# Kernel tuning notes

Measured on AMD Instinct MI355X. Metric: run time of the kernel, lower is better.

Reference implementation:

```python
import jax, jax.numpy as jnp
import numpy as np

V, E, H, L = 16384, 256, 1024, 2  # vocab, edim, rnn_size, layer_depth
B, T, S = 128, 256, 64            # batch, seq_length, nce_samples


def _xavier(k, shape):
    lim = np.sqrt(6.0 / (shape[-2] + shape[-1]))
    return jax.random.uniform(k, shape, jnp.float32, -lim, lim)


def setup_inputs() -> dict:
    key = jax.random.key(0)
    ks = jax.random.split(key, 12)
    return {
        "input_data": jax.random.randint(ks[0], (B, T), 0, V, jnp.int32),
        "targets": jax.random.randint(ks[1], (B, T), 0, V, jnp.int32),
        "nce_samples": jax.random.randint(ks[2], (S,), 0, V, jnp.int32),
        # embedding + input projection (edim != rnn_size path)
        "embedding": _xavier(ks[3], (V, E)),
        "win": _xavier(ks[4], (E, H)),
        "bin_": jnp.zeros((H,), jnp.float32),
        # MI-GRU per-layer params, stacked on leading layer dim L
        "Wxg": _xavier(ks[5], (L, H, 2 * H)),
        "Whg": _xavier(ks[6], (L, H, 2 * H)),
        "ag": jnp.ones((L, 2 * H), jnp.float32),
        "b1g": jnp.full((L, 2 * H), 0.5, jnp.float32),
        "b2g": jnp.full((L, 2 * H), 0.5, jnp.float32),
        "bg": jnp.zeros((L, 2 * H), jnp.float32),
        "Wxc": _xavier(ks[7], (L, H, H)),
        "Whc": _xavier(ks[8], (L, H, H)),
        "ac": jnp.ones((L, H), jnp.float32),
        "b1c": jnp.full((L, H), 0.5, jnp.float32),
        "b2c": jnp.full((L, H), 0.5, jnp.float32),
        "bc": jnp.zeros((L, H), jnp.float32),
        # output / NCE params
        "softmax_w": _xavier(ks[9], (V, H)),
        "softmax_b": jnp.zeros((V,), jnp.float32),
    }


def _mi_gru_stack(x_seq, h0, Wxg, Whg, ag, b1g, b2g, bg, Wxc, Whc, ac, b1c, b2c, bc):
    """x_seq: [T,B,H]; h0: [L,B,H]. Multiplicative-Integration GRU, L layers."""
    nL = h0.shape[0]

    def step(h_all, x_t):
        inp = x_t
        new_h = []
        for l in range(nL):
            h = h_all[l]
            gx = inp @ Wxg[l]                      # [B,2H]
            gh = h @ Whg[l]                        # [B,2H]
            g = jax.nn.sigmoid(ag[l] * gx * gh + b1g[l] * gx + b2g[l] * gh + bg[l])
            r, u = jnp.split(g, 2, axis=-1)        # reset, update gates [B,H]
            cx = inp @ Wxc[l]
            ch = (r * h) @ Whc[l]
            c = jnp.tanh(ac[l] * cx * ch + b1c[l] * cx + b2c[l] * ch + bc[l])
            hn = u * h + (1.0 - u) * c
            new_h.append(hn)
            inp = hn
        return jnp.stack(new_h), inp

    _, outs = jax.lax.scan(step, h0, x_seq)        # outs: [T,B,H] top-layer states
    return outs


def reference(input_data, targets, nce_samples, embedding, win, bin_,
              Wxg, Whg, ag, b1g, b2g, bg, Wxc, Whc, ac, b1c, b2c, bc,
              softmax_w, softmax_b):
    b, t = input_data.shape
    h_dim = win.shape[1]
    # embedding lookup + projection edim -> rnn_size
    emb = embedding[input_data]                            # [B,T,E]
    x = jnp.einsum('bte,eh->bth', emb, win) + bin_         # [B,T,H]
    x_seq = jnp.transpose(x, (1, 0, 2))                    # [T,B,H]
    h0 = jnp.zeros((Wxg.shape[0], b, h_dim), x.dtype)
    outs = _mi_gru_stack(x_seq, h0, Wxg, Whg, ag, b1g, b2g, bg,
                         Wxc, Whc, ac, b1c, b2c, bc)       # [T,B,H]
    out = jnp.transpose(outs, (1, 0, 2)).reshape(-1, h_dim)  # [B*T,H]
    # NCE loss with fixed sampled negatives
    labels = targets.reshape(-1)                           # [B*T]
    true_w = softmax_w[labels]                             # [B*T,H]
    true_logit = jnp.sum(true_w * out, axis=-1) + softmax_b[labels]
    samp_w = softmax_w[nce_samples]                        # [S,H]
    samp_logits = out @ samp_w.T + softmax_b[nce_samples]  # [B*T,S]
    # sigmoid cross-entropy: label 1 for true, 0 for sampled
    loss = jax.nn.softplus(-true_logit) + jnp.sum(jax.nn.softplus(samp_logits), axis=-1)
    cost = jnp.sum(loss) / b / t
    return cost
```

## Files before the change

kernel.cpp:

```cpp
#include <hip/hip_runtime.h>
#include <hip/hip_bf16.h>


#define T_SEQ 256
#define BATCH 128
#define HD    1024

typedef __attribute__((ext_vector_type(8))) short short8v;
typedef __attribute__((ext_vector_type(4))) float f32x4;

static __device__ __forceinline__ short f2b(float v) {
  __hip_bfloat16 h = __float2bfloat16(v);
  return __builtin_bit_cast(short, h);
}
static __device__ __forceinline__ float b2f(short s) {
  return __bfloat162float(__builtin_bit_cast(__hip_bfloat16, s));
}
static __device__ __forceinline__ float sigm(float x) { return 1.f / (1.f + __expf(-x)); }
static __device__ __forceinline__ float splus(float x) {
  return fmaxf(x, 0.f) + log1pf(__expf(-fabsf(x)));
}

struct Acc22 { f32x4 a[2][2]; };

static __device__ __forceinline__ void gemm_wave(
    const short* __restrict__ A, int lda, const short* __restrict__ WT, int ldk,
    int row0, int cb, int K, Acc22& o) {
  const int lane = threadIdx.x & 63;
  const int l15 = lane & 15, g = lane >> 4;
  f32x4 z = {0.f, 0.f, 0.f, 0.f};
  o.a[0][0] = z; o.a[0][1] = z; o.a[1][0] = z; o.a[1][1] = z;
  const short* a0 = A + (size_t)(row0 + l15) * lda + g * 8;
  const short* a1 = a0 + 16 * (size_t)lda;
  const short* b0 = WT + (size_t)(cb + l15) * ldk + g * 8;
  const short* b1 = b0 + 16 * (size_t)ldk;
  for (int k = 0; k < K; k += 32) {
    short8v av0 = *(const short8v*)(a0 + k);
    short8v av1 = *(const short8v*)(a1 + k);
    short8v bv0 = *(const short8v*)(b0 + k);
    short8v bv1 = *(const short8v*)(b1 + k);
    o.a[0][0] = __builtin_amdgcn_mfma_f32_16x16x32_bf16(av0, bv0, o.a[0][0], 0, 0, 0);
    o.a[0][1] = __builtin_amdgcn_mfma_f32_16x16x32_bf16(av0, bv1, o.a[0][1], 0, 0, 0);
    o.a[1][0] = __builtin_amdgcn_mfma_f32_16x16x32_bf16(av1, bv0, o.a[1][0], 0, 0, 0);
    o.a[1][1] = __builtin_amdgcn_mfma_f32_16x16x32_bf16(av1, bv1, o.a[1][1], 0, 0, 0);
  }
}

struct Params {
  const int *tok, *tgt, *nce;
  const float *emb, *win, *binp;
  const float *ag, *b1g, *b2g, *bg, *ac, *b1c, *b2c, *bc;
  const float *smw, *smb;
  short *embB, *winT, *WhgT0, *WhgT1, *WhcT0, *WhcT1, *WXC0T, *WXC1T;
  short *sampWT;
  float *sampb;
  short *X, *OUTb;
  float *h0f, *h1f; short *h0b, *h1b;
  short *rh0b, *rh1b;
  float *u0, *u1, *gh1, *cx1;
  float *gxc0a, *gxc0b;
  float *slog;
  float *dout;
};


__global__ void k_zero(float* __restrict__ p, int n, float* __restrict__ dout) {
  int i = blockIdx.x * 256 + threadIdx.x;
  if (i < n) p[i] = 0.f;
  if (blockIdx.x == 0 && threadIdx.x == 0) *dout = 0.f;
}

__global__ void k_conv(const float* __restrict__ s, short* __restrict__ d, int n) {
  int i = (blockIdx.x * 256 + threadIdx.x) * 4;
  if (i + 4 <= n) {
    float4 v = *(const float4*)(s + i);
    d[i] = f2b(v.x); d[i + 1] = f2b(v.y); d[i + 2] = f2b(v.z); d[i + 3] = f2b(v.w);
  }
}

__global__ void k_transpose(const float* __restrict__ W, short* __restrict__ WT,
                            int K, int N) {
  __shared__ short tile[32][33];
  int nt = blockIdx.x, kt = blockIdx.y;
  int tx = threadIdx.x, ty = threadIdx.y;
#pragma unroll
  for (int r = 0; r < 4; r++) {
    int k = kt * 32 + ty + r * 8;
    int n = nt * 32 + tx;
    tile[ty + r * 8][tx] = f2b(W[(size_t)k * N + n]);
  }
  __syncthreads();
#pragma unroll
  for (int r = 0; r < 4; r++) {
    int n = nt * 32 + ty + r * 8;
    int k = kt * 32 + tx;
    WT[(size_t)n * K + k] = tile[tx][ty + r * 8];
  }
}

__global__ void k_sampw(Params p) {
  int s = blockIdx.x;
  int row = p.nce[s];
  for (int j = threadIdx.x; j < HD; j += 256)
    p.sampWT[s * HD + j] = f2b(p.smw[(size_t)row * HD + j]);
  if (threadIdx.x == 0) p.sampb[s] = p.smb[row];
}

__global__ __launch_bounds__(256) void k_xproj(Params p) {
  int blk = blockIdx.x;
  int mt = blk >> 5, nt = blk & 31;
  int w = threadIdx.x >> 6, lane = threadIdx.x & 63, l15 = lane & 15, g = lane >> 4;
  int row0 = mt * 128 + w * 32, cb = nt * 32;
  const short* ap[2];
#pragma unroll
  for (int mi = 0; mi < 2; mi++) {
    int r = row0 + mi * 16 + l15;
    int tt = r >> 7, bb = r & 127;
    int tk = p.tok[bb * T_SEQ + tt];
    ap[mi] = p.embB + (size_t)tk * 256 + g * 8;
  }
  f32x4 z = {0.f, 0.f, 0.f, 0.f};
  Acc22 acc; acc.a[0][0] = z; acc.a[0][1] = z; acc.a[1][0] = z; acc.a[1][1] = z;
  const short* b0 = p.winT + (size_t)(cb + l15) * 256 + g * 8;
  const short* b1 = b0 + 16 * 256;
  for (int k = 0; k < 256; k += 32) {
    short8v av0 = *(const short8v*)(ap[0] + k);
    short8v av1 = *(const short8v*)(ap[1] + k);
    short8v bv0 = *(const short8v*)(b0 + k);
    short8v bv1 = *(const short8v*)(b1 + k);
    acc.a[0][0] = __builtin_amdgcn_mfma_f32_16x16x32_bf16(av0, bv0, acc.a[0][0], 0, 0, 0);
    acc.a[0][1] = __builtin_amdgcn_mfma_f32_16x16x32_bf16(av0, bv1, acc.a[0][1], 0, 0, 0);
    acc.a[1][0] = __builtin_amdgcn_mfma_f32_16x16x32_bf16(av1, bv0, acc.a[1][0], 0, 0, 0);
    acc.a[1][1] = __builtin_amdgcn_mfma_f32_16x16x32_bf16(av1, bv1, acc.a[1][1], 0, 0, 0);
  }
#pragma unroll
  for (int mi = 0; mi < 2; mi++)
#pragma unroll
    for (int ni = 0; ni < 2; ni++)
#pragma unroll
      for (int i = 0; i < 4; i++) {
        int row = row0 + mi * 16 + g * 4 + i;
        int col = cb + ni * 16 + l15;
        p.X[(size_t)row * HD + col] = f2b(acc.a[mi][ni][i] + p.binp[col]);
      }
}

__global__ __launch_bounds__(256) void k_gxc0init(Params p) {
  int blk = blockIdx.x;
  int w = threadIdx.x >> 6, lane = threadIdx.x & 63, l15 = lane & 15, g = lane >> 4;
  int row0 = w * 32, cb = blk * 32;
  Acc22 acc;
  gemm_wave(p.X, HD, p.WXC0T, HD, row0, cb, HD, acc);
#pragma unroll
  for (int mi = 0; mi < 2; mi++)
#pragma unroll
    for (int ni = 0; ni < 2; ni++)
#pragma unroll
      for (int i = 0; i < 4; i++) {
        int row = row0 + mi * 16 + g * 4 + i;
        int col = cb + ni * 16 + l15;
        p.gxc0a[row * 3072 + col] = acc.a[mi][ni][i];
      }
}


__global__ __launch_bounds__(256) void k_step1(Params p, int t) {
  int blk = blockIdx.x;
  int w = threadIdx.x >> 6, lane = threadIdx.x & 63, l15 = lane & 15, g = lane >> 4;
  int row0 = w * 32;
  bool L0 = blk < 64;
  int cb = (L0 ? blk : blk - 64) * 32;
  const float* gxc = (t & 1) ? p.gxc0b : p.gxc0a;
  Acc22 acc;
  gemm_wave(L0 ? p.h0b : p.h1b, HD, L0 ? p.WhgT0 : p.WhgT1, HD, row0, cb, HD, acc);
#pragma unroll
  for (int mi = 0; mi < 2; mi++)
#pragma unroll
    for (int ni = 0; ni < 2; ni++)
#pragma unroll
      for (int i = 0; i < 4; i++) {
        int row = row0 + mi * 16 + g * 4 + i;
        int col = cb + ni * 16 + l15;
        float gh = acc.a[mi][ni][i];
        if (L0) {
          float gx = gxc[row * 3072 + col];
          float gv = sigm(p.ag[col] * gx * gh + p.b1g[col] * gx + p.b2g[col] * gh + p.bg[col]);
          if (col < HD) p.rh0b[row * HD + col] = f2b(gv * p.h0f[row * HD + col]);
          else          p.u0[row * HD + col - HD] = gv;
        } else {
          p.gh1[row * 2048 + col] = gh;
        }
      }
}

__global__ __launch_bounds__(256) void k_step2(Params p, int t) {
  int blk = blockIdx.x;
  int w = threadIdx.x >> 6, lane = threadIdx.x & 63, l15 = lane & 15, g = lane >> 4;
  int row0 = w * 32, cb = blk * 32;
  const float* gxc = (t & 1) ? p.gxc0b : p.gxc0a;
  Acc22 acc;
  gemm_wave(p.rh0b, HD, p.WhcT0, HD, row0, cb, HD, acc);
#pragma unroll
  for (int mi = 0; mi < 2; mi++)
#pragma unroll
    for (int ni = 0; ni < 2; ni++)
#pragma unroll
      for (int i = 0; i < 4; i++) {
        int row = row0 + mi * 16 + g * 4 + i;
        int col = cb + ni * 16 + l15;
        float ch = acc.a[mi][ni][i];
        float cx = gxc[row * 3072 + 2048 + col];
        float cv = tanhf(p.ac[col] * cx * ch + p.b1c[col] * cx + p.b2c[col] * ch + p.bc[col]);
        float un = p.u0[row * HD + col];
        float ho = p.h0f[row * HD + col];
        float hn = un * ho + (1.f - un) * cv;
        p.h0f[row * HD + col] = hn;
        p.h0b[row * HD + col] = f2b(hn);
      }
}

__global__ __launch_bounds__(256) void k_step3(Params p, int t) {
  int blk = blockIdx.x;
  int w = threadIdx.x >> 6, lane = threadIdx.x & 63, l15 = lane & 15, g = lane >> 4;
  int row0 = w * 32, cb = blk * 32;
  Acc22 acc;
  gemm_wave(p.h0b, HD, p.WXC1T, HD, row0, cb, HD, acc);
#pragma unroll
  for (int mi = 0; mi < 2; mi++)
#pragma unroll
    for (int ni = 0; ni < 2; ni++)
#pragma unroll
      for (int i = 0; i < 4; i++) {
        int row = row0 + mi * 16 + g * 4 + i;
        int col = cb + ni * 16 + l15;
        float v = acc.a[mi][ni][i];
        if (col < 2048) {
          float gh = p.gh1[row * 2048 + col];
          float gv = sigm(p.ag[2048 + col] * v * gh + p.b1g[2048 + col] * v +
                          p.b2g[2048 + col] * gh + p.bg[2048 + col]);
          if (col < HD) p.rh1b[row * HD + col] = f2b(gv * p.h1f[row * HD + col]);
          else          p.u1[row * HD + col - HD] = gv;
        } else {
          p.cx1[row * HD + col - 2048] = v;
        }
      }
}

__global__ __launch_bounds__(256) void k_step4(Params p, int t) {
  int blk = blockIdx.x;
  int w = threadIdx.x >> 6, lane = threadIdx.x & 63, l15 = lane & 15, g = lane >> 4;
  int row0 = w * 32;
  if (blk < 32) {
    int cb = blk * 32;
    Acc22 acc;
    gemm_wave(p.rh1b, HD, p.WhcT1, HD, row0, cb, HD, acc);
#pragma unroll
    for (int mi = 0; mi < 2; mi++)
#pragma unroll
      for (int ni = 0; ni < 2; ni++)
#pragma unroll
        for (int i = 0; i < 4; i++) {
          int row = row0 + mi * 16 + g * 4 + i;
          int col = cb + ni * 16 + l15;
          float ch = acc.a[mi][ni][i];
          float cx = p.cx1[row * HD + col];
          float cv = tanhf(p.ac[HD + col] * cx * ch + p.b1c[HD + col] * cx +
                           p.b2c[HD + col] * ch + p.bc[HD + col]);
          float un = p.u1[row * HD + col];
          float ho = p.h1f[row * HD + col];
          float hn = un * ho + (1.f - un) * cv;
          p.h1f[row * HD + col] = hn;
          p.h1b[row * HD + col] = f2b(hn);
          p.OUTb[((size_t)t * BATCH + row) * HD + col] = f2b(hn);
        }
  } else {
    if (t == T_SEQ - 1) return;
    int cb = (blk - 32) * 32;
    const short* A = p.X + (size_t)(t + 1) * BATCH * HD;
    float* outb = ((t + 1) & 1) ? p.gxc0b : p.gxc0a;
    Acc22 acc;
    gemm_wave(A, HD, p.WXC0T, HD, row0, cb, HD, acc);
#pragma unroll
    for (int mi = 0; mi < 2; mi++)
#pragma unroll
      for (int ni = 0; ni < 2; ni++)
#pragma unroll
        for (int i = 0; i < 4; i++) {
          int row = row0 + mi * 16 + g * 4 + i;
          int col = cb + ni * 16 + l15;
          outb[row * 3072 + col] = acc.a[mi][ni][i];
        }
  }
}


__global__ __launch_bounds__(256) void k_nce_gemm(Params p) {
  int blk = blockIdx.x;
  int mt = blk >> 1, nt = blk & 1;
  int w = threadIdx.x >> 6, lane = threadIdx.x & 63, l15 = lane & 15, g = lane >> 4;
  int row0 = w * 32, cb = nt * 32;
  Acc22 acc;
  gemm_wave(p.OUTb + (size_t)mt * 128 * HD, HD, p.sampWT, HD, row0, cb, HD, acc);
#pragma unroll
  for (int mi = 0; mi < 2; mi++)
#pragma unroll
    for (int ni = 0; ni < 2; ni++)
#pragma unroll
      for (int i = 0; i < 4; i++) {
        int row = mt * 128 + row0 + mi * 16 + g * 4 + i;
        int col = cb + ni * 16 + l15;
        p.slog[(size_t)row * 64 + col] = acc.a[mi][ni][i] + p.sampb[col];
      }
}

__global__ __launch_bounds__(256) void k_loss(Params p) {
  __shared__ float acc4[4];
  int w = threadIdx.x >> 6, lane = threadIdx.x & 63;
  int r = blockIdx.x * 4 + w;
  int b = r >> 8, t = r & 255;
  int q = t * BATCH + b;
  int label = p.tgt[r];
  const short* orow = p.OUTb + (size_t)q * HD;
  const float4* t4 = (const float4*)(p.smw + (size_t)label * HD) + lane * 4;
  float s = 0.f;
  const short8v* o8 = (const short8v*)(orow + lane * 16);
#pragma unroll
  for (int u2 = 0; u2 < 2; u2++) {
    short8v ov = o8[u2];
    float4 ta = t4[u2 * 2], tb = t4[u2 * 2 + 1];
    s += b2f(ov[0]) * ta.x + b2f(ov[1]) * ta.y + b2f(ov[2]) * ta.z + b2f(ov[3]) * ta.w;
    s += b2f(ov[4]) * tb.x + b2f(ov[5]) * tb.y + b2f(ov[6]) * tb.z + b2f(ov[7]) * tb.w;
  }
  for (int off = 32; off; off >>= 1) s += __shfl_down(s, off);
  float tl = __shfl(s, 0) + p.smb[label];
  float sl = p.slog[(size_t)q * 64 + lane];
  float v = splus(sl);
  for (int off = 32; off; off >>= 1) v += __shfl_down(v, off);
  if (lane == 0) acc4[w] = v + splus(-tl);
  __syncthreads();
  if (threadIdx.x == 0)
    atomicAdd(p.dout, (acc4[0] + acc4[1] + acc4[2] + acc4[3]) * (1.f / 32768.f));
}


extern "C" void kernel_launch(void* const* d_in, const int* in_sizes, int n_in,
                              void* d_out, int out_size, void* d_ws, size_t ws_size,
                              hipStream_t stream) {
  Params p;
  p.tok = (const int*)d_in[0];
  p.tgt = (const int*)d_in[1];
  p.nce = (const int*)d_in[2];
  p.emb = (const float*)d_in[3];
  p.win = (const float*)d_in[4];
  p.binp = (const float*)d_in[5];
  const float* Wxg = (const float*)d_in[6];
  const float* Whg = (const float*)d_in[7];
  p.ag = (const float*)d_in[8];
  p.b1g = (const float*)d_in[9];
  p.b2g = (const float*)d_in[10];
  p.bg = (const float*)d_in[11];
  const float* Wxc = (const float*)d_in[12];
  const float* Whc = (const float*)d_in[13];
  p.ac = (const float*)d_in[14];
  p.b1c = (const float*)d_in[15];
  p.b2c = (const float*)d_in[16];
  p.bc = (const float*)d_in[17];
  p.smw = (const float*)d_in[18];
  p.smb = (const float*)d_in[19];
  p.dout = (float*)d_out;

  char* w = (char*)d_ws;
  size_t off = 0;
  auto alloc = [&](size_t bytes) -> void* {
    void* q = w + off;
    off += (bytes + 255) & ~(size_t)255;
    return q;
  };
  p.embB   = (short*)alloc((size_t)16384 * 256 * 2);
  p.winT   = (short*)alloc((size_t)1024 * 256 * 2);
  p.WhgT0  = (short*)alloc((size_t)2048 * 1024 * 2);
  p.WhgT1  = (short*)alloc((size_t)2048 * 1024 * 2);
  p.WhcT0  = (short*)alloc((size_t)1024 * 1024 * 2);
  p.WhcT1  = (short*)alloc((size_t)1024 * 1024 * 2);
  p.WXC0T  = (short*)alloc((size_t)3072 * 1024 * 2);
  p.WXC1T  = (short*)alloc((size_t)3072 * 1024 * 2);
  p.sampWT = (short*)alloc((size_t)64 * 1024 * 2);
  p.sampb  = (float*)alloc(64 * 4);
  p.X      = (short*)alloc((size_t)32768 * 1024 * 2);
  p.OUTb   = (short*)alloc((size_t)32768 * 1024 * 2);
  p.h0f    = (float*)alloc((size_t)BATCH * HD * 4);
  p.h1f    = (float*)alloc((size_t)BATCH * HD * 4);
  p.h0b    = (short*)alloc((size_t)BATCH * HD * 2);
  p.h1b    = (short*)alloc((size_t)BATCH * HD * 2);
  p.rh0b   = (short*)alloc((size_t)BATCH * HD * 2);
  p.rh1b   = (short*)alloc((size_t)BATCH * HD * 2);
  p.u0     = (float*)alloc((size_t)BATCH * HD * 4);
  p.u1     = (float*)alloc((size_t)BATCH * HD * 4);
  p.gh1    = (float*)alloc((size_t)BATCH * 2048 * 4);
  p.cx1    = (float*)alloc((size_t)BATCH * HD * 4);
  p.gxc0a  = (float*)alloc((size_t)BATCH * 3072 * 4);
  p.gxc0b  = (float*)alloc((size_t)BATCH * 3072 * 4);
  p.slog   = (float*)alloc((size_t)32768 * 64 * 4);

  k_zero<<<1536, 256, 0, stream>>>(p.h0f, 393216, p.dout);
  k_conv<<<4096, 256, 0, stream>>>(p.emb, p.embB, 16384 * 256);
  dim3 tb(32, 8);
  k_transpose<<<dim3(32, 8),  tb, 0, stream>>>(p.win, p.winT, 256, 1024);
  k_transpose<<<dim3(64, 32), tb, 0, stream>>>(Whg, p.WhgT0, 1024, 2048);
  k_transpose<<<dim3(64, 32), tb, 0, stream>>>(Whg + (size_t)1024 * 2048, p.WhgT1, 1024, 2048);
  k_transpose<<<dim3(32, 32), tb, 0, stream>>>(Whc, p.WhcT0, 1024, 1024);
  k_transpose<<<dim3(32, 32), tb, 0, stream>>>(Whc + (size_t)1024 * 1024, p.WhcT1, 1024, 1024);
  k_transpose<<<dim3(64, 32), tb, 0, stream>>>(Wxg, p.WXC0T, 1024, 2048);
  k_transpose<<<dim3(32, 32), tb, 0, stream>>>(Wxc, p.WXC0T + (size_t)2048 * 1024, 1024, 1024);
  k_transpose<<<dim3(64, 32), tb, 0, stream>>>(Wxg + (size_t)1024 * 2048, p.WXC1T, 1024, 2048);
  k_transpose<<<dim3(32, 32), tb, 0, stream>>>(Wxc + (size_t)1024 * 1024, p.WXC1T + (size_t)2048 * 1024, 1024, 1024);
  k_sampw<<<64, 256, 0, stream>>>(p);
  k_xproj<<<8192, 256, 0, stream>>>(p);
  k_gxc0init<<<96, 256, 0, stream>>>(p);

  for (int t = 0; t < T_SEQ; t++) {
    k_step1<<<128, 256, 0, stream>>>(p, t);
    k_step2<<<32, 256, 0, stream>>>(p, t);
    k_step3<<<96, 256, 0, stream>>>(p, t);
    k_step4<<<128, 256, 0, stream>>>(p, t);
  }

  k_nce_gemm<<<512, 256, 0, stream>>>(p);
  k_loss<<<8192, 256, 0, stream>>>(p);
}
```

Before: 23.27 ms.

## Replace per-timestep kernel launches with persistent recurrent kernel using grid barriers

```diff
diff --git a/kernel.cpp b/kernel.cpp
--- a/kernel.cpp
+++ b/kernel.cpp
@@ -5,6 +5,7 @@
 #define T_SEQ 256
 #define BATCH 128
 #define HD    1024
+#define NBLK  256
 
 typedef __attribute__((ext_vector_type(8))) short short8v;
 typedef __attribute__((ext_vector_type(4))) float f32x4;
@@ -46,6 +47,20 @@
   }
 }
 
+static __device__ __forceinline__ f32x4 tile16(const short* __restrict__ A,
+    const short* __restrict__ BT, int cb, int arow, int l15, int g8) {
+  f32x4 acc = {0.f, 0.f, 0.f, 0.f};
+  const short* ap = A + (size_t)arow * HD + g8;
+  const short* bp = BT + (size_t)(cb + l15) * HD + g8;
+#pragma unroll 8
+  for (int ks = 0; ks < 32; ++ks) {
+    short8v av = *(const short8v*)(ap + ks * 32);
+    short8v bv = *(const short8v*)(bp + ks * 32);
+    acc = __builtin_amdgcn_mfma_f32_16x16x32_bf16(av, bv, acc, 0, 0, 0);
+  }
+  return acc;
+}
+
 struct Params {
   const int *tok, *tgt, *nce;
   const float *emb, *win, *binp;
@@ -57,17 +72,42 @@
   short *X, *OUTb;
   float *h0f, *h1f; short *h0b, *h1b;
   short *rh0b, *rh1b;
-  float *u0, *u1, *gh1, *cx1;
+  float *u0, *u1, *cx1;
   float *gxc0a, *gxc0b;
   float *slog;
   float *dout;
 };
 
-
-__global__ void k_zero(float* __restrict__ p, int n, float* __restrict__ dout) {
+static __device__ __forceinline__ void gbar(int* bar) {
+  __syncthreads();
+  if (threadIdx.x == 0) {
+    __threadfence();
+    int* rgen = bar + 64;
+    int g0 = __hip_atomic_load(rgen, __ATOMIC_RELAXED, __HIP_MEMORY_SCOPE_AGENT);
+    int* gcnt = bar + 128 + (blockIdx.x >> 4) * 64;
+    if (__hip_atomic_fetch_add(gcnt, 1, __ATOMIC_ACQ_REL, __HIP_MEMORY_SCOPE_AGENT) == 15) {
+      __hip_atomic_store(gcnt, 0, __ATOMIC_RELAXED, __HIP_MEMORY_SCOPE_AGENT);
+      if (__hip_atomic_fetch_add(bar, 1, __ATOMIC_ACQ_REL, __HIP_MEMORY_SCOPE_AGENT) == 15) {
+        __hip_atomic_store(bar, 0, __ATOMIC_RELAXED, __HIP_MEMORY_SCOPE_AGENT);
+        __hip_atomic_store(rgen, g0 + 1, __ATOMIC_RELEASE, __HIP_MEMORY_SCOPE_AGENT);
+      }
+    }
+    while (__hip_atomic_load(rgen, __ATOMIC_ACQUIRE, __HIP_MEMORY_SCOPE_AGENT) == g0)
+      __builtin_amdgcn_s_sleep(2);
+  }
+  __syncthreads();
+  __threadfence();
+}
+
+
+__global__ void k_zero(float* __restrict__ p, int n, float* __restrict__ dout,
+                       int* __restrict__ bar) {
   int i = blockIdx.x * 256 + threadIdx.x;
   if (i < n) p[i] = 0.f;
-  if (blockIdx.x == 0 && threadIdx.x == 0) *dout = 0.f;
+  if (blockIdx.x == 0) {
+    for (int j = threadIdx.x; j < 2048; j += 256) bar[j] = 0;
+    if (threadIdx.x == 0) *dout = 0.f;
+  }
 }
 
 __global__ void k_conv(const float* __restrict__ s, short* __restrict__ d, int n) {
@@ -163,133 +203,106 @@
       }
 }
 
-
-__global__ __launch_bounds__(256) void k_step1(Params p, int t) {
-  int blk = blockIdx.x;
-  int w = threadIdx.x >> 6, lane = threadIdx.x & 63, l15 = lane & 15, g = lane >> 4;
-  int row0 = w * 32;
-  bool L0 = blk < 64;
-  int cb = (L0 ? blk : blk - 64) * 32;
-  const float* gxc = (t & 1) ? p.gxc0b : p.gxc0a;
-  Acc22 acc;
-  gemm_wave(L0 ? p.h0b : p.h1b, HD, L0 ? p.WhgT0 : p.WhgT1, HD, row0, cb, HD, acc);
-#pragma unroll
-  for (int mi = 0; mi < 2; mi++)
-#pragma unroll
-    for (int ni = 0; ni < 2; ni++)
-#pragma unroll
-      for (int i = 0; i < 4; i++) {
-        int row = row0 + mi * 16 + g * 4 + i;
-        int col = cb + ni * 16 + l15;
-        float gh = acc.a[mi][ni][i];
-        if (L0) {
-          float gx = gxc[row * 3072 + col];
-          float gv = sigm(p.ag[col] * gx * gh + p.b1g[col] * gx + p.b2g[col] * gh + p.bg[col]);
-          if (col < HD) p.rh0b[row * HD + col] = f2b(gv * p.h0f[row * HD + col]);
-          else          p.u0[row * HD + col - HD] = gv;
-        } else {
-          p.gh1[row * 2048 + col] = gh;
+__global__ __launch_bounds__(512, 2) void k_recur(Params p, int* bar) {
+  const int blk = blockIdx.x;
+  const int tid = threadIdx.x;
+  const int w = tid >> 6, lane = tid & 63, l15 = lane & 15, g = lane >> 4;
+  const int arow = w * 16 + l15;
+  const int g8 = g * 8;
+  const int rbase = w * 16 + g * 4;
+
+  for (int s = 0; s <= T_SEQ; ++s) {
+    const float* gxc_s = (s & 1) ? p.gxc0b : p.gxc0a;
+    if (blk < 128) {
+      if (s >= 1) {
+        int cb = blk * 16;
+        f32x4 x1 = tile16(p.h0b, p.WXC1T, cb, arow, l15, g8);
+        f32x4 h1g = tile16(p.h1b, p.WhgT1, cb, arow, l15, g8);
+        int c = cb + l15;
+#pragma unroll
+        for (int i = 0; i < 4; ++i) {
+          int r = rbase + i;
+          float gv = sigm(p.ag[2048 + c] * x1[i] * h1g[i] + p.b1g[2048 + c] * x1[i] +
+                          p.b2g[2048 + c] * h1g[i] + p.bg[2048 + c]);
+          if (c < HD) p.rh1b[r * HD + c] = f2b(gv * p.h1f[r * HD + c]);
+          else        p.u1[r * HD + c - HD] = gv;
         }
       }
-}
-
-__global__ __launch_bounds__(256) void k_step2(Params p, int t) {
-  int blk = blockIdx.x;
-  int w = threadIdx.x >> 6, lane = threadIdx.x & 63, l15 = lane & 15, g = lane >> 4;
-  int row0 = w * 32, cb = blk * 32;
-  const float* gxc = (t & 1) ? p.gxc0b : p.gxc0a;
-  Acc22 acc;
-  gemm_wave(p.rh0b, HD, p.WhcT0, HD, row0, cb, HD, acc);
-#pragma unroll
-  for (int mi = 0; mi < 2; mi++)
-#pragma unroll
-    for (int ni = 0; ni < 2; ni++)
-#pragma unroll
-      for (int i = 0; i < 4; i++) {
-        int row = row0 + mi * 16 + g * 4 + i;
-        int col = cb + ni * 16 + l15;
-        float ch = acc.a[mi][ni][i];
-        float cx = gxc[row * 3072 + 2048 + col];
-        float cv = tanhf(p.ac[col] * cx * ch + p.b1c[col] * cx + p.b2c[col] * ch + p.bc[col]);
-        float un = p.u0[row * HD + col];
-        float ho = p.h0f[row * HD + col];
-        float hn = un * ho + (1.f - un) * cv;
-        p.h0f[row * HD + col] = hn;
-        p.h0b[row * HD + col] = f2b(hn);
-      }
-}
-
-__global__ __launch_bounds__(256) void k_step3(Params p, int t) {
-  int blk = blockIdx.x;
-  int w = threadIdx.x >> 6, lane = threadIdx.x & 63, l15 = lane & 15, g = lane >> 4;
-  int row0 = w * 32, cb = blk * 32;
-  Acc22 acc;
-  gemm_wave(p.h0b, HD, p.WXC1T, HD, row0, cb, HD, acc);
-#pragma unroll
-  for (int mi = 0; mi < 2; mi++)
-#pragma unroll
-    for (int ni = 0; ni < 2; ni++)
-#pragma unroll
-      for (int i = 0; i < 4; i++) {
-        int row = row0 + mi * 16 + g * 4 + i;
-        int col = cb + ni * 16 + l15;
-        float v = acc.a[mi][ni][i];
-        if (col < 2048) {
-          float gh = p.gh1[row * 2048 + col];
-          float gv = sigm(p.ag[2048 + col] * v * gh + p.b1g[2048 + col] * v +
-                          p.b2g[2048 + col] * gh + p.bg[2048 + col]);
-          if (col < HD) p.rh1b[row * HD + col] = f2b(gv * p.h1f[row * HD + col]);
-          else          p.u1[row * HD + col - HD] = gv;
-        } else {
-          p.cx1[row * HD + col - 2048] = v;
+    } else {
+      if (s < T_SEQ) {
+        int cb = (blk - 128) * 16;
+        f32x4 gh = tile16(p.h0b, p.WhgT0, cb, arow, l15, g8);
+        int c = cb + l15;
+#pragma unroll
+        for (int i = 0; i < 4; ++i) {
+          int r = rbase + i;
+          float gx = gxc_s[r * 3072 + c];
+          float gv = sigm(p.ag[c] * gx * gh[i] + p.b1g[c] * gx +
+                          p.b2g[c] * gh[i] + p.bg[c]);
+          if (c < HD) p.rh0b[r * HD + c] = f2b(gv * p.h0f[r * HD + c]);
+          else        p.u0[r * HD + c - HD] = gv;
         }
       }
-}
-
-__global__ __launch_bounds__(256) void k_step4(Params p, int t) {
-  int blk = blockIdx.x;
-  int w = threadIdx.x >> 6, lane = threadIdx.x & 63, l15 = lane & 15, g = lane >> 4;
-  int row0 = w * 32;
-  if (blk < 32) {
-    int cb = blk * 32;
-    Acc22 acc;
-    gemm_wave(p.rh1b, HD, p.WhcT1, HD, row0, cb, HD, acc);
-#pragma unroll
-    for (int mi = 0; mi < 2; mi++)
-#pragma unroll
-      for (int ni = 0; ni < 2; ni++)
-#pragma unroll
-        for (int i = 0; i < 4; i++) {
-          int row = row0 + mi * 16 + g * 4 + i;
-          int col = cb + ni * 16 + l15;
-          float ch = acc.a[mi][ni][i];
-          float cx = p.cx1[row * HD + col];
-          float cv = tanhf(p.ac[HD + col] * cx * ch + p.b1c[HD + col] * cx +
-                           p.b2c[HD + col] * ch + p.bc[HD + col]);
-          float un = p.u1[row * HD + col];
-          float ho = p.h1f[row * HD + col];
-          float hn = un * ho + (1.f - un) * cv;
-          p.h1f[row * HD + col] = hn;
-          p.h1b[row * HD + col] = f2b(hn);
-          p.OUTb[((size_t)t * BATCH + row) * HD + col] = f2b(hn);
+      if (blk < 192 && s >= 1) {
+        int cb2 = (blk - 128) * 16;
+        f32x4 cx = tile16(p.h0b, p.WXC1T, 2048 + cb2, arow, l15, g8);
+        int c = cb2 + l15;
+#pragma unroll
+        for (int i = 0; i < 4; ++i) p.cx1[(rbase + i) * HD + c] = cx[i];
+      }
+    }
+    gbar(bar);
+    float* gxc_n = ((s + 1) & 1) ? p.gxc0b : p.gxc0a;
+    if (blk < 64) {
+      if (s < T_SEQ) {
+        int cb = blk * 16;
+        f32x4 ch = tile16(p.rh0b, p.WhcT0, cb, arow, l15, g8);
+        int c = cb + l15;
+#pragma unroll
+        for (int i = 0; i < 4; ++i) {
+          int r = rbase + i;
+          float cx = gxc_s[r * 3072 + 2048 + c];
+          float cv = tanhf(p.ac[c] * cx * ch[i] + p.b1c[c] * cx +
+                           p.b2c[c] * ch[i] + p.bc[c]);
+          float un = p.u0[r * HD + c];
+          float hn = un * p.h0f[r * HD + c] + (1.f - un) * cv;
+          p.h0f[r * HD + c] = hn;
+          p.h0b[r * HD + c] = f2b(hn);
         }
-  } else {
-    if (t == T_SEQ - 1) return;
-    int cb = (blk - 32) * 32;
-    const short* A = p.X + (size_t)(t + 1) * BATCH * HD;
-    float* outb = ((t + 1) & 1) ? p.gxc0b : p.gxc0a;
-    Acc22 acc;
-    gemm_wave(A, HD, p.WXC0T, HD, row0, cb, HD, acc);
-#pragma unroll
-    for (int mi = 0; mi < 2; mi++)
-#pragma unroll
-      for (int ni = 0; ni < 2; ni++)
-#pragma unroll
-        for (int i = 0; i < 4; i++) {
-          int row = row0 + mi * 16 + g * 4 + i;
-          int col = cb + ni * 16 + l15;
-          outb[row * 3072 + col] = acc.a[mi][ni][i];
+      }
+      if (s + 1 < T_SEQ) {
+        int cb = (128 + blk) * 16;
+        f32x4 v = tile16(p.X + (size_t)(s + 1) * BATCH * HD, p.WXC0T, cb, arow, l15, g8);
+#pragma unroll
+        for (int i = 0; i < 4; ++i) gxc_n[(rbase + i) * 3072 + cb + l15] = v[i];
+      }
+    } else if (blk < 128) {
+      if (s >= 1) {
+        int cb = (blk - 64) * 16;
+        f32x4 ch = tile16(p.rh1b, p.WhcT1, cb, arow, l15, g8);
+        int c = cb + l15;
+#pragma unroll
+        for (int i = 0; i < 4; ++i) {
+          int r = rbase + i;
+          float cx = p.cx1[r * HD + c];
+          float cv = tanhf(p.ac[HD + c] * cx * ch[i] + p.b1c[HD + c] * cx +
+                           p.b2c[HD + c] * ch[i] + p.bc[HD + c]);
+          float un = p.u1[r * HD + c];
+          float hn = un * p.h1f[r * HD + c] + (1.f - un) * cv;
+          p.h1f[r * HD + c] = hn;
+          p.h1b[r * HD + c] = f2b(hn);
+          p.OUTb[((size_t)(s - 1) * BATCH + r) * HD + c] = f2b(hn);
         }
+      }
+    } else {
+      if (s + 1 < T_SEQ) {
+        int cb = (blk - 128) * 16;
+        f32x4 v = tile16(p.X + (size_t)(s + 1) * BATCH * HD, p.WXC0T, cb, arow, l15, g8);
+#pragma unroll
+        for (int i = 0; i < 4; ++i) gxc_n[(rbase + i) * 3072 + cb + l15] = v[i];
+      }
+    }
+    gbar(bar);
   }
 }
 
@@ -396,13 +409,13 @@
   p.rh1b   = (short*)alloc((size_t)BATCH * HD * 2);
   p.u0     = (float*)alloc((size_t)BATCH * HD * 4);
   p.u1     = (float*)alloc((size_t)BATCH * HD * 4);
-  p.gh1    = (float*)alloc((size_t)BATCH * 2048 * 4);
   p.cx1    = (float*)alloc((size_t)BATCH * HD * 4);
   p.gxc0a  = (float*)alloc((size_t)BATCH * 3072 * 4);
   p.gxc0b  = (float*)alloc((size_t)BATCH * 3072 * 4);
   p.slog   = (float*)alloc((size_t)32768 * 64 * 4);
-
-  k_zero<<<1536, 256, 0, stream>>>(p.h0f, 393216, p.dout);
+  int* bar = (int*)alloc(8192);
+
+  k_zero<<<1536, 256, 0, stream>>>(p.h0f, 393216, p.dout, bar);
   k_conv<<<4096, 256, 0, stream>>>(p.emb, p.embB, 16384 * 256);
   dim3 tb(32, 8);
   k_transpose<<<dim3(32, 8),  tb, 0, stream>>>(p.win, p.winT, 256, 1024);
@@ -418,12 +431,7 @@
   k_xproj<<<8192, 256, 0, stream>>>(p);
   k_gxc0init<<<96, 256, 0, stream>>>(p);
 
-  for (int t = 0; t < T_SEQ; t++) {
-    k_step1<<<128, 256, 0, stream>>>(p, t);
-    k_step2<<<32, 256, 0, stream>>>(p, t);
-    k_step3<<<96, 256, 0, stream>>>(p, t);
-    k_step4<<<128, 256, 0, stream>>>(p, t);
-  }
+  k_recur<<<NBLK, 512, 0, stream>>>(p, bar);
 
   k_nce_gemm<<<512, 256, 0, stream>>>(p);
   k_loss<<<8192, 256, 0, stream>>>(p);
```

New measurement: 53.29 ms. +129.0%, slower.
